# Kernel tuning notes

Hardware: AMD Instinct MI355X
Metric: run time of the kernel (lower is better)

## Reference

```python
import jax, jax.numpy as jnp
import numpy as np

# ---- config (mirrors cfg / init kwargs) ----
FEAT_STRIDE = 16
IM_DIMS = (1024, 1024)          # (height, width)
ANCHOR_SCALES = (8, 16, 32)
ANCHOR_RATIOS = (0.5, 1.0, 2.0)
PRE_NMS_TOPN = 6000             # eval mode (cfg_key=1)
POST_NMS_TOPN = 300
NMS_THRESH = 0.7
MIN_SIZE = 16


def _generate_base_anchors(base_size=16, ratios=ANCHOR_RATIOS, scales=ANCHOR_SCALES):
    """py-faster-rcnn generate_anchors, in numpy (static)."""
    def mk(ws, hs, xc, yc):
        return np.stack([xc - 0.5 * (ws - 1), yc - 0.5 * (hs - 1),
                         xc + 0.5 * (ws - 1), yc + 0.5 * (hs - 1)], axis=1)
    base = np.array([0, 0, base_size - 1, base_size - 1], dtype=np.float64)
    w = base[2] - base[0] + 1; h = base[3] - base[1] + 1
    xc = base[0] + 0.5 * (w - 1); yc = base[1] + 0.5 * (h - 1)
    # ratio enum
    size = w * h
    ws = np.round(np.sqrt(size / np.array(ratios)))
    hs = np.round(ws * np.array(ratios))
    ratio_anchors = mk(ws, hs, xc, yc)
    # scale enum
    out = []
    for a in ratio_anchors:
        aw = a[2] - a[0] + 1; ah = a[3] - a[1] + 1
        axc = a[0] + 0.5 * (aw - 1); ayc = a[1] + 0.5 * (ah - 1)
        out.append(mk(aw * np.array(scales), ah * np.array(scales), axc, ayc))
    return np.concatenate(out, axis=0).astype(np.float32)  # [A,4]


def _all_anchors(H, W):
    base = _generate_base_anchors()                       # [A,4]
    sx = np.arange(W) * FEAT_STRIDE
    sy = np.arange(H) * FEAT_STRIDE
    sx, sy = np.meshgrid(sx, sy)
    shifts = np.stack([sx.ravel(), sy.ravel(), sx.ravel(), sy.ravel()], axis=1)  # [H*W,4]
    anchors = shifts[:, None, :].astype(np.float32) + base[None, :, :]
    return anchors.reshape(-1, 4)                         # [H*W*A, 4]


def setup_inputs() -> dict:
    key = jax.random.key(0)
    k1, k2 = jax.random.split(key)
    H, W, A = 64, 64, 9
    rpn_cls_score = jax.random.normal(k1, (1, H, W, 2 * A), dtype=jnp.float32)
    rpn_bbox_pred = jax.random.normal(k2, (1, H, W, 4 * A), dtype=jnp.float32)
    return {"rpn_cls_score": rpn_cls_score, "rpn_bbox_pred": rpn_bbox_pred}


def _proposals(rpn_cls_score, rpn_bbox_pred):
    _, H, W, C2 = rpn_cls_score.shape
    A = C2 // 2
    # rpn_softmax: per-anchor 2-way softmax, foreground prob
    scores = jax.nn.softmax(rpn_cls_score.reshape(H, W, A, 2), axis=-1)[..., 1].reshape(-1)  # [N]
    deltas = rpn_bbox_pred.reshape(-1, 4)                  # [N,4]
    anchors = jnp.asarray(_all_anchors(H, W))              # [N,4]
    # bbox_transform_inv
    aw = anchors[:, 2] - anchors[:, 0] + 1.0
    ah = anchors[:, 3] - anchors[:, 1] + 1.0
    axc = anchors[:, 0] + 0.5 * aw
    ayc = anchors[:, 1] + 0.5 * ah
    dx, dy, dw, dh = deltas[:, 0], deltas[:, 1], deltas[:, 2], deltas[:, 3]
    pxc = dx * aw + axc; pyc = dy * ah + ayc
    pw = jnp.exp(dw) * aw; ph = jnp.exp(dh) * ah
    x1 = pxc - 0.5 * pw; y1 = pyc - 0.5 * ph
    x2 = pxc + 0.5 * pw; y2 = pyc + 0.5 * ph
    # clip to image
    im_h, im_w = IM_DIMS
    x1 = jnp.clip(x1, 0.0, im_w - 1.0); x2 = jnp.clip(x2, 0.0, im_w - 1.0)
    y1 = jnp.clip(y1, 0.0, im_h - 1.0); y2 = jnp.clip(y2, 0.0, im_h - 1.0)
    boxes = jnp.stack([x1, y1, x2, y2], axis=1)            # [N,4]
    # filter too-small boxes by masking their score
    valid = ((x2 - x1 + 1.0) >= MIN_SIZE) & ((y2 - y1 + 1.0) >= MIN_SIZE)
    scores = jnp.where(valid, scores, -jnp.inf)
    return boxes, scores


def _nms_keep(boxes, K):
    """Greedy NMS keep-mask over score-descending boxes [K,4]."""
    x1, y1, x2, y2 = boxes[:, 0], boxes[:, 1], boxes[:, 2], boxes[:, 3]
    areas = (x2 - x1 + 1.0) * (y2 - y1 + 1.0)
    ix1 = jnp.maximum(x1[:, None], x1[None, :])
    iy1 = jnp.maximum(y1[:, None], y1[None, :])
    ix2 = jnp.minimum(x2[:, None], x2[None, :])
    iy2 = jnp.minimum(y2[:, None], y2[None, :])
    iw = jnp.maximum(ix2 - ix1 + 1.0, 0.0)
    ih = jnp.maximum(iy2 - iy1 + 1.0, 0.0)
    inter = iw * ih
    iou = inter / (areas[:, None] + areas[None, :] - inter)  # [K,K]
    idxs = jnp.arange(K)
    def body(i, keep):
        sup = keep[i] & (iou[i] > NMS_THRESH) & (idxs > i)
        return keep & ~sup
    return jax.lax.fori_loop(0, K, body, jnp.ones((K,), bool))


def reference(rpn_cls_score, rpn_bbox_pred):
    boxes, scores = _proposals(rpn_cls_score, rpn_bbox_pred)
    K = min(PRE_NMS_TOPN, scores.shape[0])
    top_scores, order = jax.lax.top_k(scores, K)           # score-descending
    top_boxes = boxes[order]                               # [K,4]
    keep = _nms_keep(top_boxes, K)
    sel_scores = jnp.where(keep, top_scores, -jnp.inf)
    _, idx = jax.lax.top_k(sel_scores, POST_NMS_TOPN)      # kept, in score order
    out_boxes = top_boxes[idx]                             # [post,4]
    blob = jnp.concatenate([jnp.zeros((POST_NMS_TOPN, 1), out_boxes.dtype), out_boxes], axis=1)
    return blob                                            # [post,5] (batch_idx, x1,y1,x2,y2)
```

## Files before the change

kernel.cpp:

```cpp
#include <hip/hip_runtime.h>
#include <stdint.h>

typedef unsigned long long u64;
typedef unsigned int u32;

#define N_ANCH 36864
#define WGRID 64
#define A_PER 9
#define KTOP 6000
#define NOUT 300
#define NBIN 5120
#define NCHK 94
#define NJ   6016
#define INF_BIN 0
#define PCAP 6

__constant__ float c_ax1[9] = {-84.f,-176.f,-360.f,-56.f,-120.f,-248.f,-36.f,-80.f,-168.f};
__constant__ float c_ay1[9] = {-40.f,-88.f,-184.f,-56.f,-120.f,-248.f,-80.f,-168.f,-344.f};
__constant__ float c_aw[9]  = {184.f,368.f,736.f,128.f,256.f,512.f,88.f,176.f,352.f};
__constant__ float c_ah[9]  = {96.f,192.f,384.f,128.f,256.f,512.f,176.f,352.f,704.f};

__device__ __forceinline__ u32 binof(u32 u) {
    if (u < 0x80000000u) return 0u;
    if (u < 0xBF000000u) return 1u + ((u - 0x80000000u) >> 22);
    return 256u + ((u - 0xBF000000u) >> 11);
}

__global__ __launch_bounds__(256) void proposal_kernel(const float* __restrict__ cls,
                                                       const float* __restrict__ dlt,
                                                       u64* __restrict__ keys,
                                                       float4* __restrict__ boxes,
                                                       u32* __restrict__ hist) {
    __shared__ u32 lh[NBIN];
    const int t = threadIdx.x;
    for (int b = t; b < NBIN; b += 256) lh[b] = 0;
    __syncthreads();

    int i = blockIdx.x * 256 + t;
    int a  = i % A_PER;
    int hw = i / A_PER;
    int wx = hw % WGRID;
    int hy = hw / WGRID;

    float2 lp = *(const float2*)(cls + hw * 18 + 2 * a);
    float l0 = lp.x, l1 = lp.y;
    float m  = fmaxf(l0, l1);
    float e0 = expf(l0 - m), e1 = expf(l1 - m);
    float s  = e1 / (e0 + e1);

    float4 dd = *(const float4*)(dlt + hw * 36 + 4 * a);
    float dx = dd.x, dy = dd.y, dw = dd.z, dh = dd.w;
    float aw = c_aw[a], ah = c_ah[a];
    float axc = (c_ax1[a] + 16.f * (float)wx) + 0.5f * aw;
    float ayc = (c_ay1[a] + 16.f * (float)hy) + 0.5f * ah;

    float pxc = dx * aw + axc;
    float pyc = dy * ah + ayc;
    float pw  = expf(dw) * aw;
    float ph  = expf(dh) * ah;
    float x1 = pxc - 0.5f * pw, y1 = pyc - 0.5f * ph;
    float x2 = pxc + 0.5f * pw, y2 = pyc + 0.5f * ph;
    x1 = fminf(fmaxf(x1, 0.f), 1023.f);
    x2 = fminf(fmaxf(x2, 0.f), 1023.f);
    y1 = fminf(fmaxf(y1, 0.f), 1023.f);
    y2 = fminf(fmaxf(y2, 0.f), 1023.f);
    bool valid = ((x2 - x1 + 1.f) >= 16.f) && ((y2 - y1 + 1.f) >= 16.f);
    float sc = valid ? s : -__builtin_huge_valf();

    u32 sb  = __float_as_uint(sc);
    u32 ord = (sb & 0x80000000u) ? ~sb : (sb | 0x80000000u);
    u64 key = ((u64)ord << 32) | (u32)(~(u32)i);
    keys[i]  = key;
    boxes[i] = make_float4(x1, y1, x2, y2);

    u64 infb = __ballot(!valid);
    if (valid) {
        atomicAdd(&lh[binof(ord)], 1u);
    } else {
        int lane = t & 63;
        if (lane == __builtin_ctzll(infb))
            atomicAdd(&lh[INF_BIN], (u32)__popcll(infb));
    }
    __syncthreads();
    for (int b = t; b < NBIN; b += 256) {
        u32 v = lh[b];
        if (v) atomicAdd(&hist[b], v);
    }
}

__global__ __launch_bounds__(1024) void scan_kernel(const u32* __restrict__ hist,
                                                    u32* __restrict__ binStart,
                                                    u32* __restrict__ gEV) {
    __shared__ u32 sh[1024];
    int t = threadIdx.x;
    if (t == 0) gEV[1] = KTOP;
    int hi = NBIN - 1 - 5 * t;
    u32 cnt[5];
    u32 sum = 0;
#pragma unroll
    for (int k = 0; k < 5; ++k) { cnt[k] = hist[hi - k]; sum += cnt[k]; }
    sh[t] = sum;
    __syncthreads();
    for (int d = 1; d < 1024; d <<= 1) {
        u32 v = (t >= d) ? sh[t - d] : 0;
        __syncthreads();
        sh[t] += v;
        __syncthreads();
    }
    u32 run = sh[t] - sum;
#pragma unroll
    for (int k = 0; k < 5; ++k) {
        int b = hi - k;
        binStart[b] = run;
        u32 end = run + cnt[k];
        if (run < KTOP && end >= KTOP) gEV[0] = end;
        run = end;
    }
}

__global__ void scatter_kernel(const u64* __restrict__ keys,
                               const u32* __restrict__ binStart,
                               u32* __restrict__ cursor,
                               u64* __restrict__ scat) {
    int i = blockIdx.x * blockDim.x + threadIdx.x;
    if (i >= N_ANCH) return;
    u64 k = keys[i];
    u32 b = binof((u32)(k >> 32));
    u32 s = binStart[b];
    if (s < KTOP) {
        u32 p = s + atomicAdd(&cursor[b], 1u);
        scat[p] = k;
    }
}

__global__ void rank_kernel(const u64* __restrict__ scat,
                            const u32* __restrict__ binStart,
                            const u32* __restrict__ hist,
                            const float4* __restrict__ boxes,
                            const u32* __restrict__ gEV,
                            float4* __restrict__ topBoxes,
                            int* __restrict__ gV) {
    int i = blockIdx.x * blockDim.x + threadIdx.x;
    u32 E = gEV[0];
    if (i >= (int)E) return;
    u64 k = scat[i];
    u32 b = binof((u32)(k >> 32));
    u32 s = binStart[b], c = hist[b];
    u32 r = s;
    for (u32 j = s; j < s + c; ++j) r += (scat[j] > k) ? 1u : 0u;
    if (r < KTOP) {
        int idx = (int)(~(u32)k);
        topBoxes[r] = boxes[idx];
        if (!(k >> 63)) atomicMin(gV, (int)r);
    }
}

__device__ __forceinline__ bool iou_gt(float4 a, float areaA, float4 b, float areaB) {
    float ix1 = fmaxf(a.x, b.x), iy1 = fmaxf(a.y, b.y);
    float ix2 = fminf(a.z, b.z), iy2 = fminf(a.w, b.w);
    float iw = fmaxf(ix2 - ix1 + 1.0f, 0.0f);
    float ih = fmaxf(iy2 - iy1 + 1.0f, 0.0f);
    float inter = iw * ih;
    float iou = inter / (areaA + areaB - inter);
    return iou > 0.7f;
}

__global__ __launch_bounds__(256) void maskT_kernel(const float4* __restrict__ topBoxes,
                                                    const u32* __restrict__ gEV,
                                                    u64* __restrict__ S) {
    const int V = (int)gEV[1];
    const int nch = (V + 63) >> 6;
    const int jc = blockIdx.x;
    const int w0 = blockIdx.y * 4;
    if (jc >= nch || w0 > jc) return;
    __shared__ float4 cb[256];
    __shared__ float  ca[256];
    const int t = threadIdx.x;
    const int lane = t & 63;
    {
        int ci = w0 * 64 + t;
        float4 b = (ci < V) ? topBoxes[ci] : make_float4(0.f, 0.f, -8.f, -8.f);
        cb[t] = b;
        ca[t] = (b.z - b.x + 1.f) * (b.w - b.y + 1.f);
    }
    __syncthreads();
    const int w = w0 + (t >> 6);
    if (w > jc || w >= nch) return;
    const int j = jc * 64 + lane;
    float4 bj = (j < V) ? topBoxes[j] : make_float4(0.f, 0.f, -8.f, -8.f);
    float aj = (bj.z - bj.x + 1.f) * (bj.w - bj.y + 1.f);
    const int s0 = (t >> 6) * 64;
    u64 m = 0;
#pragma unroll 4
    for (int b = 0; b < 64; ++b)
        if (iou_gt(bj, aj, cb[s0 + b], ca[s0 + b])) m |= (1ull << b);
    if (w == jc) m &= ((1ull << lane) - 1ull);
    S[(u64)w * NJ + j] = m;
}

__global__ __launch_bounds__(1024) void nms_out_kernel(const float4* __restrict__ topBoxes,
                                                       const u32* __restrict__ gEV,
                                                       const u64* __restrict__ S,
                                                       float* __restrict__ out) {
    __shared__ u64 keepw[NCHK];
    __shared__ u64 supw[16];
    __shared__ u32 scanbuf[1024];
    __shared__ int s_nkept;
    const int t = threadIdx.x;
    const int lane = t & 63;
    const int v = t >> 6;
    if (t < NCHK) keepw[t] = 0;
    if (t == 0) s_nkept = 0;
    const int V = (int)gEV[1];
    const int nch = (V + 63) >> 6;

    u64 kw[PCAP], pendE[PCAP], pendO[PCAP];
#pragma unroll
    for (int k = 0; k < PCAP; ++k) { kw[k] = 0; pendE[k] = 0; pendO[k] = 0; }
    u64 dtE = 0, dtO = 0;
#pragma unroll
    for (int k = 0; k < PCAP; ++k) {
        int w = v + 16 * k;
        if (w < 1 && 1 < nch) pendO[k] = S[(u64)w * NJ + 64 + lane];
    }
    if (v == 0) {
        dtE = S[lane];
        if (nch > 1) dtO = S[(u64)NJ + 64 + lane];
    }
    __syncthreads();

    for (int c = 0; c < nch; ++c) {
        if (s_nkept >= NOUT) break;
#pragma unroll
        for (int k = 0; k < PCAP; ++k) {
            int w = v + 16 * k;
            if (w == c - 1) kw[k] = keepw[w];
        }
        u64 acc = 0;
        if (c & 1) {
#pragma unroll
            for (int k = 0; k < PCAP; ++k) { int w = v + 16 * k; if (w < c) acc |= pendO[k] & kw[k]; }
        } else {
#pragma unroll
            for (int k = 0; k < PCAP; ++k) { int w = v + 16 * k; if (w < c) acc |= pendE[k] & kw[k]; }
        }
        u64 bal = __ballot(acc != 0ull);
        if (lane == 0) supw[v] = bal;
        const int cn = c + 2;
        if (cn < nch) {
            const u64* Sc = S + (u64)cn * 64 + lane;
            if (c & 1) {
#pragma unroll
                for (int k = 0; k < PCAP; ++k) { int w = v + 16 * k; if (w < cn) pendO[k] = Sc[(u64)w * NJ]; }
            } else {
#pragma unroll
                for (int k = 0; k < PCAP; ++k) { int w = v + 16 * k; if (w < cn) pendE[k] = Sc[(u64)w * NJ]; }
            }
        }
        __syncthreads();
        if (v == 0) {
            u64 sup = 0;
#pragma unroll
            for (int q = 0; q < 16; ++q) sup |= supw[q];
            int rem = V - c * 64;
            u64 aliveM = (rem >= 64) ? ~0ull : ((1ull << rem) - 1ull);
            u64 cand = ~sup & aliveM;
            u64 dT = (c & 1) ? dtO : dtE;
            u64 kb = 0;
            while (cand) {
                int b = __builtin_ctzll(cand);
                kb |= (1ull << b);
                cand &= ~(1ull << b);
                cand &= ~__ballot(((dT >> b) & 1ull) != 0ull);
            }
            if (lane == 0) { keepw[c] = kb; s_nkept += __popcll(kb); }
            if (cn < nch) {
                u64 dload = S[(u64)cn * NJ + (u64)cn * 64 + lane];
                if (c & 1) dtO = dload; else dtE = dload;
            }
        }
        __syncthreads();
    }
    __syncthreads();

    const int per = 6;
    int r0 = t * per;
    int r1 = min(r0 + per, KTOP);
    u32 cnt = 0;
    for (int r = r0; r < r1; ++r)
        cnt += (u32)((keepw[r >> 6] >> (r & 63)) & 1ull);
    scanbuf[t] = cnt;
    __syncthreads();
    for (int d = 1; d < 1024; d <<= 1) {
        u32 vv = (t >= d) ? scanbuf[t - d] : 0;
        __syncthreads();
        scanbuf[t] += vv;
        __syncthreads();
    }
    const int total = (int)scanbuf[1023];
    const int n1 = min(total, NOUT);
    int kp = (int)(scanbuf[t] - cnt);
    for (int r = r0; r < r1; ++r) {
        int kept = (int)((keepw[r >> 6] >> (r & 63)) & 1ull);
        int pos = kept ? kp : (n1 + r - kp);
        if (pos < NOUT) {
            float4 b = topBoxes[r];
            out[pos * 5 + 0] = 0.f;
            out[pos * 5 + 1] = b.x;
            out[pos * 5 + 2] = b.y;
            out[pos * 5 + 3] = b.z;
            out[pos * 5 + 4] = b.w;
        }
        kp += kept;
    }
}

extern "C" void kernel_launch(void* const* d_in, const int* in_sizes, int n_in,
                              void* d_out, int out_size, void* d_ws, size_t ws_size,
                              hipStream_t stream) {
    const float* cls = (const float*)d_in[0];
    const float* dlt = (const float*)d_in[1];
    float* out = (float*)d_out;
    char* ws = (char*)d_ws;
    u64*    keys     = (u64*)   (ws);
    u64*    scat     = (u64*)   (ws + 294912);
    float4* boxes    = (float4*)(ws + 589824);
    float4* topBoxes = (float4*)(ws + 1179648);
    u32*    hist     = (u32*)   (ws + 1275648);
    u32*    cursor   = (u32*)   (ws + 1296128);
    u32*    binStart = (u32*)   (ws + 1316608);
    u32*    gEV      = (u32*)   (ws + 1337088);
    u64*    S        = (u64*)   (ws + 1337344);

    hipMemsetAsync(hist, 0, 2 * NBIN * sizeof(u32), stream);
    proposal_kernel<<<144, 256, 0, stream>>>(cls, dlt, keys, boxes, hist);
    scan_kernel<<<1, 1024, 0, stream>>>(hist, binStart, gEV);
    scatter_kernel<<<(N_ANCH + 255) / 256, 256, 0, stream>>>(keys, binStart, cursor, scat);
    rank_kernel<<<(N_ANCH + 255) / 256, 256, 0, stream>>>(scat, binStart, hist, boxes, gEV,
                                                          topBoxes, (int*)&gEV[1]);
    maskT_kernel<<<dim3(NCHK, (NCHK + 3) / 4), 256, 0, stream>>>(topBoxes, gEV, S);
    nms_out_kernel<<<1, 1024, 0, stream>>>(topBoxes, gEV, S, out);
}
```

Measured before the change: 121.0 us.

## Replicate NMS chunk resolution across waves and use wave-shuffle scans

Result: slower. 131.3 us (+8.5%).

```diff
diff --git a/kernel.cpp b/kernel.cpp
--- a/kernel.cpp
+++ b/kernel.cpp
@@ -14,6 +14,12 @@
 #define NJ   6016
 #define INF_BIN 0
 #define PCAP 6
+
+#define BARRIER_LDS() do {                                   \
+    asm volatile("s_waitcnt lgkmcnt(0)" ::: "memory");       \
+    __builtin_amdgcn_s_barrier();                            \
+    asm volatile("" ::: "memory");                           \
+} while (0)
 
 __constant__ float c_ax1[9] = {-84.f,-176.f,-360.f,-56.f,-120.f,-248.f,-36.f,-80.f,-168.f};
 __constant__ float c_ay1[9] = {-40.f,-88.f,-184.f,-56.f,-120.f,-248.f,-80.f,-168.f,-344.f};
@@ -91,23 +97,31 @@
 __global__ __launch_bounds__(1024) void scan_kernel(const u32* __restrict__ hist,
                                                     u32* __restrict__ binStart,
                                                     u32* __restrict__ gEV) {
-    __shared__ u32 sh[1024];
-    int t = threadIdx.x;
+    __shared__ u32 wsum[16];
+    const int t = threadIdx.x;
+    const int lane = t & 63;
+    const int v = t >> 6;
     if (t == 0) gEV[1] = KTOP;
     int hi = NBIN - 1 - 5 * t;
     u32 cnt[5];
     u32 sum = 0;
 #pragma unroll
     for (int k = 0; k < 5; ++k) { cnt[k] = hist[hi - k]; sum += cnt[k]; }
-    sh[t] = sum;
-    __syncthreads();
-    for (int d = 1; d < 1024; d <<= 1) {
-        u32 v = (t >= d) ? sh[t - d] : 0;
-        __syncthreads();
-        sh[t] += v;
-        __syncthreads();
-    }
-    u32 run = sh[t] - sum;
+    u32 s = sum;
+#pragma unroll
+    for (int d = 1; d < 64; d <<= 1) {
+        u32 x = __shfl_up(s, d, 64);
+        if (lane >= d) s += x;
+    }
+    if (lane == 63) wsum[v] = s;
+    __syncthreads();
+    u32 base = 0;
+#pragma unroll
+    for (int q = 0; q < 16; ++q) {
+        u32 x = wsum[q];
+        if (q < v) base += x;
+    }
+    u32 run = base + s - sum;
 #pragma unroll
     for (int k = 0; k < 5; ++k) {
         int b = hi - k;
@@ -203,14 +217,12 @@
                                                        const u64* __restrict__ S,
                                                        float* __restrict__ out) {
     __shared__ u64 keepw[NCHK];
-    __shared__ u64 supw[16];
-    __shared__ u32 scanbuf[1024];
-    __shared__ int s_nkept;
+    __shared__ u64 supw[2][16];
+    __shared__ u32 wsum[16];
     const int t = threadIdx.x;
     const int lane = t & 63;
     const int v = t >> 6;
     if (t < NCHK) keepw[t] = 0;
-    if (t == 0) s_nkept = 0;
     const int V = (int)gEV[1];
     const int nch = (V + 63) >> 6;
 
@@ -223,21 +235,14 @@
         int w = v + 16 * k;
         if (w < 1 && 1 < nch) pendO[k] = S[(u64)w * NJ + 64 + lane];
     }
-    if (v == 0) {
-        dtE = S[lane];
-        if (nch > 1) dtO = S[(u64)NJ + 64 + lane];
-    }
-    __syncthreads();
+    dtE = S[lane];
+    if (nch > 1) dtO = S[(u64)NJ + 64 + lane];
+    int nkept = 0;
 
     for (int c = 0; c < nch; ++c) {
-        if (s_nkept >= NOUT) break;
-#pragma unroll
-        for (int k = 0; k < PCAP; ++k) {
-            int w = v + 16 * k;
-            if (w == c - 1) kw[k] = keepw[w];
-        }
+        const int par = c & 1;
         u64 acc = 0;
-        if (c & 1) {
+        if (par) {
 #pragma unroll
             for (int k = 0; k < PCAP; ++k) { int w = v + 16 * k; if (w < c) acc |= pendO[k] & kw[k]; }
         } else {
@@ -245,11 +250,11 @@
             for (int k = 0; k < PCAP; ++k) { int w = v + 16 * k; if (w < c) acc |= pendE[k] & kw[k]; }
         }
         u64 bal = __ballot(acc != 0ull);
-        if (lane == 0) supw[v] = bal;
+        if (lane == 0) supw[par][v] = bal;
         const int cn = c + 2;
         if (cn < nch) {
             const u64* Sc = S + (u64)cn * 64 + lane;
-            if (c & 1) {
+            if (par) {
 #pragma unroll
                 for (int k = 0; k < PCAP; ++k) { int w = v + 16 * k; if (w < cn) pendO[k] = Sc[(u64)w * NJ]; }
             } else {
@@ -257,29 +262,31 @@
                 for (int k = 0; k < PCAP; ++k) { int w = v + 16 * k; if (w < cn) pendE[k] = Sc[(u64)w * NJ]; }
             }
         }
-        __syncthreads();
-        if (v == 0) {
-            u64 sup = 0;
-#pragma unroll
-            for (int q = 0; q < 16; ++q) sup |= supw[q];
-            int rem = V - c * 64;
-            u64 aliveM = (rem >= 64) ? ~0ull : ((1ull << rem) - 1ull);
-            u64 cand = ~sup & aliveM;
-            u64 dT = (c & 1) ? dtO : dtE;
-            u64 kb = 0;
-            while (cand) {
-                int b = __builtin_ctzll(cand);
-                kb |= (1ull << b);
-                cand &= ~(1ull << b);
-                cand &= ~__ballot(((dT >> b) & 1ull) != 0ull);
-            }
-            if (lane == 0) { keepw[c] = kb; s_nkept += __popcll(kb); }
-            if (cn < nch) {
-                u64 dload = S[(u64)cn * NJ + (u64)cn * 64 + lane];
-                if (c & 1) dtO = dload; else dtE = dload;
-            }
-        }
-        __syncthreads();
+        BARRIER_LDS();
+        u64 sup = 0;
+#pragma unroll
+        for (int q = 0; q < 16; ++q) sup |= supw[par][q];
+        int rem = V - c * 64;
+        u64 aliveM = (rem >= 64) ? ~0ull : ((1ull << rem) - 1ull);
+        u64 cand = ~sup & aliveM;
+        u64 dT = par ? dtO : dtE;
+        u64 kb = 0;
+        while (cand) {
+            int b = __builtin_ctzll(cand);
+            kb |= (1ull << b);
+            cand &= ~(1ull << b);
+            cand &= ~__ballot(((dT >> b) & 1ull) != 0ull);
+        }
+        if (t == 0) keepw[c] = kb;
+        if (cn < nch) {
+            u64 dload = S[(u64)cn * NJ + (u64)cn * 64 + lane];
+            if (par) dtO = dload; else dtE = dload;
+        }
+#pragma unroll
+        for (int k = 0; k < PCAP; ++k)
+            if (v + 16 * k == c) kw[k] = kb;
+        nkept += __popcll(kb);
+        if (nkept >= NOUT) break;
     }
     __syncthreads();
 
@@ -289,17 +296,24 @@
     u32 cnt = 0;
     for (int r = r0; r < r1; ++r)
         cnt += (u32)((keepw[r >> 6] >> (r & 63)) & 1ull);
-    scanbuf[t] = cnt;
-    __syncthreads();
-    for (int d = 1; d < 1024; d <<= 1) {
-        u32 vv = (t >= d) ? scanbuf[t - d] : 0;
-        __syncthreads();
-        scanbuf[t] += vv;
-        __syncthreads();
-    }
-    const int total = (int)scanbuf[1023];
-    const int n1 = min(total, NOUT);
-    int kp = (int)(scanbuf[t] - cnt);
+    u32 s = cnt;
+#pragma unroll
+    for (int d = 1; d < 64; d <<= 1) {
+        u32 x = __shfl_up(s, d, 64);
+        if (lane >= d) s += x;
+    }
+    if (lane == 63) wsum[v] = s;
+    __syncthreads();
+    u32 base = 0;
+    u32 total = 0;
+#pragma unroll
+    for (int q = 0; q < 16; ++q) {
+        u32 x = wsum[q];
+        if (q < v) base += x;
+        total += x;
+    }
+    const int n1 = min((int)total, NOUT);
+    int kp = (int)(base + s - cnt);
     for (int r = r0; r < r1; ++r) {
         int kept = (int)((keepw[r >> 6] >> (r & 63)) & 1ull);
         int pos = kept ? kp : (n1 + r - kp);
```
